# Kernel optimization log

Hardware: AMD Instinct MI355X
Metric: run time of the kernel (lower is better)

## Reference

```python
import jax, jax.numpy as jnp
import numpy as np

NUM_EXPERTS = 8
TOP_K = 2


def setup_inputs() -> dict:
    key = jax.random.key(0)
    ks = jax.random.split(key, 8)
    B = 16384
    D = 1024
    feat0 = jax.random.normal(ks[0], (B, 768), dtype=jnp.float32)
    feat1 = jax.random.normal(ks[1], (B, 512), dtype=jnp.float32)
    feat2 = jax.random.normal(ks[2], (B, 256), dtype=jnp.float32)
    # parameters (scaled like torch default init ~1/sqrt(fan_in))
    W_shared = jax.random.normal(ks[3], (1536, D), dtype=jnp.float32) * (1.0 / np.sqrt(1536))
    b_shared = jnp.zeros((D,), dtype=jnp.float32)
    W_gate = jax.random.normal(ks[4], (D, NUM_EXPERTS), dtype=jnp.float32) * (1.0 / np.sqrt(D))
    b_gate = jnp.zeros((NUM_EXPERTS,), dtype=jnp.float32)
    W_experts = jax.random.normal(ks[5], (NUM_EXPERTS, D, D), dtype=jnp.float32) * (1.0 / np.sqrt(D))
    b_experts = jnp.zeros((NUM_EXPERTS, D), dtype=jnp.float32)
    return {
        "feat0": feat0, "feat1": feat1, "feat2": feat2,
        "W_shared": W_shared, "b_shared": b_shared,
        "W_gate": W_gate, "b_gate": b_gate,
        "W_experts": W_experts, "b_experts": b_experts,
    }


def _moe_forward(feat0, feat1, feat2, W_shared, b_shared, W_gate, b_gate, W_experts, b_experts):
    x = jnp.concatenate([feat0, feat1, feat2], axis=1)          # (B, sum_d)
    h = jax.nn.gelu(x @ W_shared + b_shared, approximate=False)  # (B, D)
    gate_probs = jax.nn.softmax(h @ W_gate + b_gate, axis=-1)    # (B, E)
    topk_probs, topk_idx = jax.lax.top_k(gate_probs, TOP_K)      # (B, K)
    out = jnp.zeros_like(h)
    for e in range(NUM_EXPERTS):
        # per-token combine weight for expert e (0 if not routed to e)
        w_e = jnp.sum(topk_probs * (topk_idx == e), axis=1)      # (B,)
        expert_out = jax.nn.gelu(h @ W_experts[e] + b_experts[e], approximate=False)
        out = out + w_e[:, None] * expert_out
    return out


def reference(feat0, feat1, feat2, W_shared, b_shared, W_gate, b_gate, W_experts, b_experts):
    return _moe_forward(feat0, feat1, feat2, W_shared, b_shared, W_gate, b_gate, W_experts, b_experts)
```

## Files before the change

### kernel.cpp

```cpp
#include <hip/hip_runtime.h>
#include <math.h>

#define NB_TOK 16384
#define DM     1024
#define NEXP   8
#define KIN    1536

typedef __attribute__((ext_vector_type(8))) short          short8;
typedef __attribute__((ext_vector_type(8))) unsigned short ushort8;
typedef __attribute__((ext_vector_type(4))) unsigned short ushort4v;
typedef __attribute__((ext_vector_type(8))) _Float16       half8;
typedef __attribute__((ext_vector_type(4))) float          floatx4;

#define AS1U(p) ((const __attribute__((address_space(1))) unsigned int*)(p))
#define AS3U(p) ((__attribute__((address_space(3))) unsigned int*)(p))

__device__ __forceinline__ float gelu_f(float x) {
    return 0.5f * x * (1.0f + erff(x * 0.70710678118654752440f));
}

__device__ __forceinline__ unsigned short f2bf(float x) {
    unsigned u = __float_as_uint(x);
    u = (u + 0x7FFF + ((u >> 16) & 1)) >> 16;
    return (unsigned short)u;
}

__device__ __forceinline__ void split_h16(float x, unsigned short& hi, unsigned short& lo) {
    _Float16 h = (_Float16)x;
    float r = x - (float)h;
    _Float16 l = (_Float16)r;
    hi = *(unsigned short*)&h;
    lo = *(unsigned short*)&l;
}

__global__ __launch_bounds__(256) void k_splitA(
    const float* __restrict__ f0, const float* __restrict__ f1,
    const float* __restrict__ f2, unsigned short* __restrict__ Ah,
    unsigned short* __restrict__ Al)
{
    const int i4  = blockIdx.x * 256 + threadIdx.x;
    const int tok = i4 / (KIN / 4);
    const int k   = (i4 % (KIN / 4)) * 4;
    const float* src; int ld, c;
    if (k < 768)       { src = f0; ld = 768; c = k; }
    else if (k < 1280) { src = f1; ld = 512; c = k - 768; }
    else               { src = f2; ld = 256; c = k - 1280; }
    const float4 v = *(const float4*)(src + (size_t)tok * ld + c);
    const float* vp = (const float*)&v;
    ushort4v hi, lo;
#pragma unroll
    for (int j = 0; j < 4; ++j) {
        unsigned short h, l;
        split_h16(vp[j] * 4.0f, h, l);
        hi[j] = h; lo[j] = l;
    }
    *(ushort4v*)(Ah + (size_t)tok * KIN + k) = hi;
    *(ushort4v*)(Al + (size_t)tok * KIN + k) = lo;
}

__global__ __launch_bounds__(256) void k_splitB(
    const float* __restrict__ Ws, unsigned short* __restrict__ BhT,
    unsigned short* __restrict__ BlT)
{
    __shared__ float s[32][33];
    const int n0 = blockIdx.x * 32, k0 = blockIdx.y * 32;
    const int c  = threadIdx.x & 31, r = threadIdx.x >> 5;
#pragma unroll
    for (int p = 0; p < 4; ++p)
        s[r + p * 8][c] = Ws[(size_t)(k0 + r + p * 8) * DM + n0 + c];
    __syncthreads();
#pragma unroll
    for (int p = 0; p < 4; ++p) {
        const int n = r + p * 8;
        unsigned short h, l;
        split_h16(s[c][n] * 256.0f, h, l);
        BhT[(size_t)(n0 + n) * KIN + k0 + c] = h;
        BlT[(size_t)(n0 + n) * KIN + k0 + c] = l;
    }
}

__global__ __launch_bounds__(256) void k_shared_mfma(
    const unsigned short* __restrict__ Ah, const unsigned short* __restrict__ Al,
    const unsigned short* __restrict__ BhT, const unsigned short* __restrict__ BlT,
    const float* __restrict__ bs, float* __restrict__ h,
    unsigned short* __restrict__ hbf)
{
    __shared__ unsigned short ldsAh[128][64];
    __shared__ unsigned short ldsAl[128][64];
    __shared__ unsigned short ldsBh[128][64];
    __shared__ unsigned short ldsBl[128][64];

    const int t    = threadIdx.x;
    const int lane = t & 63;
    const int wave = t >> 6;
    const int row0 = blockIdx.y * 128;
    const int n0g  = blockIdx.x * 128;

    const int srow = t >> 3;
    const int g    = (t & 7) ^ (srow & 7);
    const unsigned short *sAh[4], *sAl[4], *sBh[4], *sBl[4];
#pragma unroll
    for (int q = 0; q < 4; ++q) {
        const size_t ra = (size_t)(row0 + q * 32 + srow) * KIN + g * 8;
        const size_t rb = (size_t)(n0g + q * 32 + srow) * KIN + g * 8;
        sAh[q] = Ah + ra; sAl[q] = Al + ra;
        sBh[q] = BhT + rb; sBl[q] = BlT + rb;
    }

    const int grp = lane >> 4;
    int offA[2][4], offB[2][4];
#pragma unroll
    for (int ks = 0; ks < 2; ++ks)
#pragma unroll
        for (int m = 0; m < 4; ++m) {
            const int rA = ((wave >> 1) * 64) + m * 16 + (lane & 15);
            const int rB = ((wave & 1) * 64) + m * 16 + (lane & 15);
            const int c  = ks * 4 + grp;
            offA[ks][m] = rA * 128 + (((c ^ (rA & 7)) & 7) << 4);
            offB[ks][m] = rB * 128 + (((c ^ (rB & 7)) & 7) << 4);
        }

    floatx4 acc[4][4];
#pragma unroll
    for (int m = 0; m < 4; ++m)
#pragma unroll
        for (int n = 0; n < 4; ++n) acc[m][n] = (floatx4){0.f, 0.f, 0.f, 0.f};

    const char* lAh = (const char*)&ldsAh[0][0];
    const char* lAl = (const char*)&ldsAl[0][0];
    const char* lBh = (const char*)&ldsBh[0][0];
    const char* lBl = (const char*)&ldsBl[0][0];

    for (int kt = 0; kt < KIN / 64; ++kt) {
        const int k0 = kt * 64;
        __syncthreads();
#pragma unroll
        for (int q = 0; q < 4; ++q) {
            const int dst = q * 4096 + wave * 1024;
            __builtin_amdgcn_global_load_lds(AS1U(sAh[q] + k0), AS3U((char*)lAh + dst), 16, 0, 0);
            __builtin_amdgcn_global_load_lds(AS1U(sAl[q] + k0), AS3U((char*)lAl + dst), 16, 0, 0);
            __builtin_amdgcn_global_load_lds(AS1U(sBh[q] + k0), AS3U((char*)lBh + dst), 16, 0, 0);
            __builtin_amdgcn_global_load_lds(AS1U(sBl[q] + k0), AS3U((char*)lBl + dst), 16, 0, 0);
        }
        __syncthreads();
#pragma unroll
        for (int ks = 0; ks < 2; ++ks) {
            half8 ah[4], al[4], bh[4], bl[4];
#pragma unroll
            for (int m = 0; m < 4; ++m) {
                ah[m] = *(const half8*)(lAh + offA[ks][m]);
                al[m] = *(const half8*)(lAl + offA[ks][m]);
            }
#pragma unroll
            for (int n = 0; n < 4; ++n) {
                bh[n] = *(const half8*)(lBh + offB[ks][n]);
                bl[n] = *(const half8*)(lBl + offB[ks][n]);
            }
#pragma unroll
            for (int m = 0; m < 4; ++m)
#pragma unroll
                for (int n = 0; n < 4; ++n) {
                    acc[m][n] = __builtin_amdgcn_mfma_f32_16x16x32_f16(ah[m], bh[n], acc[m][n], 0, 0, 0);
                    acc[m][n] = __builtin_amdgcn_mfma_f32_16x16x32_f16(ah[m], bl[n], acc[m][n], 0, 0, 0);
                    acc[m][n] = __builtin_amdgcn_mfma_f32_16x16x32_f16(al[m], bh[n], acc[m][n], 0, 0, 0);
                }
        }
    }

    const int wr = wave >> 1, wc = wave & 1;
#pragma unroll
    for (int n = 0; n < 4; ++n) {
        const int col  = n0g + wc * 64 + n * 16 + (lane & 15);
        const float bias = bs[col];
#pragma unroll
        for (int m = 0; m < 4; ++m) {
            const int rbase = row0 + wr * 64 + m * 16 + (lane >> 4) * 4;
#pragma unroll
            for (int reg = 0; reg < 4; ++reg) {
                const float o = gelu_f(acc[m][n][reg] * (1.0f / 1024.0f) + bias);
                h[(size_t)(rbase + reg) * DM + col]   = o;
                hbf[(size_t)(rbase + reg) * DM + col] = f2bf(o);
            }
        }
    }
}

__global__ __launch_bounds__(256) void k_wt_bf16(
    const float* __restrict__ We, unsigned short* __restrict__ WeT)
{
    __shared__ float s[32][33];
    const int e  = blockIdx.z;
    const int k0 = blockIdx.y * 32, n0 = blockIdx.x * 32;
    const int c  = threadIdx.x & 31, r = threadIdx.x >> 5;
    const float* W = We + ((size_t)e << 20);
#pragma unroll
    for (int p = 0; p < 4; ++p) {
        const int k = r + p * 8;
        s[k][c] = W[(size_t)(k0 + k) * DM + n0 + c];
    }
    __syncthreads();
#pragma unroll
    for (int p = 0; p < 4; ++p) {
        const int n = r + p * 8;
        WeT[((size_t)e << 20) + (size_t)(n0 + n) * DM + k0 + c] = f2bf(s[c][n]);
    }
}

__global__ __launch_bounds__(256) void k_gate_topk(
    const float* __restrict__ h, const float* __restrict__ Wg,
    const float* __restrict__ bg, int* __restrict__ eidx,
    float2* __restrict__ w01)
{
    const int lane = threadIdx.x & 63;
    const int wv   = threadIdx.x >> 6;
    const int tok  = blockIdx.x * 4 + wv;
    const float* hr = h + (size_t)tok * DM;
    float acc[NEXP];
#pragma unroll
    for (int e = 0; e < NEXP; ++e) acc[e] = 0.f;
    for (int j = 0; j < DM / 64; ++j) {
        const float hv = hr[lane + 64 * j];
        const float* wr = Wg + (size_t)(lane + 64 * j) * NEXP;
#pragma unroll
        for (int e = 0; e < NEXP; ++e) acc[e] = fmaf(hv, wr[e], acc[e]);
    }
#pragma unroll
    for (int off = 32; off > 0; off >>= 1) {
#pragma unroll
        for (int e = 0; e < NEXP; ++e) acc[e] += __shfl_xor(acc[e], off, 64);
    }
    if (lane == 0) {
        float lg[NEXP];
        float mx = -1e30f;
#pragma unroll
        for (int e = 0; e < NEXP; ++e) { lg[e] = acc[e] + bg[e]; mx = fmaxf(mx, lg[e]); }
        float p[NEXP]; float s = 0.f;
#pragma unroll
        for (int e = 0; e < NEXP; ++e) { p[e] = expf(lg[e] - mx); s += p[e]; }
        const float inv = 1.f / s;
        int i0 = 0;
#pragma unroll
        for (int e = 1; e < NEXP; ++e) if (p[e] > p[i0]) i0 = e;
        int i1 = (i0 == 0) ? 1 : 0;
#pragma unroll
        for (int e = 0; e < NEXP; ++e) if (e != i0 && p[e] > p[i1]) i1 = e;
        eidx[tok] = i0 | (i1 << 8);
        w01[tok]  = make_float2(p[i0] * inv, p[i1] * inv);
    }
}

__global__ __launch_bounds__(256) void k_bucket(
    const int* __restrict__ eidx, const float2* __restrict__ w01,
    int* __restrict__ counts, int* __restrict__ btok, float* __restrict__ bwgt,
    int2* __restrict__ tokslot)
{
    __shared__ int lcnt[NEXP], lbase[NEXP];
    const int tid = threadIdx.x;
    const int tok = blockIdx.x * 256 + tid;
    if (tid < NEXP) lcnt[tid] = 0;
    __syncthreads();
    const int ee = eidx[tok];
    const float2 w = w01[tok];
    const int e0 = ee & 0xff, e1 = ee >> 8;
    const int l0 = atomicAdd(&lcnt[e0], 1);
    const int l1 = atomicAdd(&lcnt[e1], 1);
    __syncthreads();
    if (tid < NEXP) lbase[tid] = atomicAdd(&counts[tid], lcnt[tid]);
    __syncthreads();
    const int s0 = lbase[e0] + l0;
    btok[e0 * NB_TOK + s0] = tok;  bwgt[e0 * NB_TOK + s0] = w.x;
    const int s1 = lbase[e1] + l1;
    btok[e1 * NB_TOK + s1] = tok;  bwgt[e1 * NB_TOK + s1] = w.y;
    tokslot[tok] = make_int2((e0 << 16) | s0, (e1 << 16) | s1);
}

__global__ void k_prefix(const int* __restrict__ counts, int* __restrict__ basep)
{
    if (threadIdx.x == 0) {
        int r = 0;
#pragma unroll
        for (int e = 0; e < NEXP; ++e) { basep[e] = r; r += counts[e]; }
    }
}

#define EXP_STAGE(b, k0)                                                                              \
    {                                                                                                 \
        char* lAw = (char*)&ldsA[b][0][0];                                                            \
        char* lBw = (char*)&ldsB[b][0][0];                                                            \
        _Pragma("unroll")                                                                             \
        for (int q = 0; q < 4; ++q) {                                                                 \
            __builtin_amdgcn_global_load_lds(AS1U(srcA[q] + (k0)), AS3U(lAw + q * 4096 + wave * 1024), 16, 0, 0); \
            __builtin_amdgcn_global_load_lds(AS1U(srcB[q] + (k0)), AS3U(lBw + q * 4096 + wave * 1024), 16, 0, 0); \
        }                                                                                             \
    }

__global__ __launch_bounds__(256) void k_expert_mfma(
    const unsigned short* __restrict__ hbf,
    const unsigned short* __restrict__ WeT,
    const float* __restrict__ bexp,
    const int* __restrict__ counts, const int* __restrict__ basep,
    const int* __restrict__ btok, const float* __restrict__ bwgt,
    float* __restrict__ stage)
{
    const int e    = blockIdx.z;
    const int cnt  = counts[e];
    const int row0 = blockIdx.y * 128;
    if (row0 >= cnt) return;
    const int gb   = basep[e];

    __shared__ unsigned short ldsA[2][128][64];
    __shared__ unsigned short ldsB[2][128][64];
    __shared__ int   sTok[128];
    __shared__ float sWt[128];

    const int t    = threadIdx.x;
    const int lane = t & 63;
    const int wave = t >> 6;

    if (t < 128) {
        const int idx = row0 + t;
        if (idx < cnt) { sTok[t] = btok[e * NB_TOK + idx]; sWt[t] = bwgt[e * NB_TOK + idx]; }
        else           { sTok[t] = -1;                     sWt[t] = 0.f; }
    }
    __syncthreads();

    const int srow = t >> 3;
    const int g    = (t & 7) ^ (srow & 7);
    const int n0g  = blockIdx.x * 128;
    const unsigned short* srcA[4];
    const unsigned short* srcB[4];
#pragma unroll
    for (int q = 0; q < 4; ++q) {
        int tk = sTok[q * 32 + srow];
        if (tk < 0) tk = 0;
        srcA[q] = hbf + (size_t)tk * DM + g * 8;
        srcB[q] = WeT + ((size_t)e << 20) + (size_t)(n0g + q * 32 + srow) * DM + g * 8;
    }

    const int grp = lane >> 4;
    int offA[2][4], offB[2][4];
#pragma unroll
    for (int ks = 0; ks < 2; ++ks)
#pragma unroll
        for (int m = 0; m < 4; ++m) {
            const int rA = ((wave >> 1) * 64) + m * 16 + (lane & 15);
            const int rB = ((wave & 1) * 64) + m * 16 + (lane & 15);
            const int c  = ks * 4 + grp;
            offA[ks][m] = rA * 128 + (((c ^ (rA & 7)) & 7) << 4);
            offB[ks][m] = rB * 128 + (((c ^ (rB & 7)) & 7) << 4);
        }

    floatx4 acc[4][4];
#pragma unroll
    for (int m = 0; m < 4; ++m)
#pragma unroll
        for (int n = 0; n < 4; ++n) acc[m][n] = (floatx4){0.f, 0.f, 0.f, 0.f};

    EXP_STAGE(0, 0);

    int buf = 0;
    for (int kt = 0; kt < DM / 64; ++kt) {
        __syncthreads();
        if (kt + 1 < DM / 64) EXP_STAGE(buf ^ 1, (kt + 1) * 64);
        const char* lA = (const char*)&ldsA[buf][0][0];
        const char* lB = (const char*)&ldsB[buf][0][0];
#pragma unroll
        for (int ks = 0; ks < 2; ++ks) {
            short8 av[4], bv[4];
#pragma unroll
            for (int m = 0; m < 4; ++m) av[m] = *(const short8*)(lA + offA[ks][m]);
#pragma unroll
            for (int n = 0; n < 4; ++n) bv[n] = *(const short8*)(lB + offB[ks][n]);
#pragma unroll
            for (int m = 0; m < 4; ++m)
#pragma unroll
                for (int n = 0; n < 4; ++n)
                    acc[m][n] = __builtin_amdgcn_mfma_f32_16x16x32_bf16(av[m], bv[n], acc[m][n], 0, 0, 0);
        }
        buf ^= 1;
    }

    const int wr = wave >> 1, wc = wave & 1;
#pragma unroll
    for (int n = 0; n < 4; ++n) {
        const int col  = n0g + wc * 64 + n * 16 + (lane & 15);
        const float bias = bexp[e * DM + col];
#pragma unroll
        for (int m = 0; m < 4; ++m) {
            const int rbase = wr * 64 + m * 16 + (lane >> 4) * 4;
#pragma unroll
            for (int reg = 0; reg < 4; ++reg) {
                const int r = rbase + reg;
                if (sTok[r] < 0) continue;
                const float v = gelu_f(acc[m][n][reg] + bias) * sWt[r];
                stage[(size_t)(gb + row0 + r) * DM + col] = v;
            }
        }
    }
}

__global__ __launch_bounds__(256) void k_combine(
    const float* __restrict__ stage, const int2* __restrict__ tokslot,
    const int* __restrict__ basep, float* __restrict__ out)
{
    const int tok = blockIdx.x;
    const int c   = threadIdx.x * 4;
    const int2 ts = tokslot[tok];
    const int g0 = basep[ts.x >> 16] + (ts.x & 0xFFFF);
    const int g1 = basep[ts.y >> 16] + (ts.y & 0xFFFF);
    const float4 a = *(const float4*)(stage + (size_t)g0 * DM + c);
    const float4 b = *(const float4*)(stage + (size_t)g1 * DM + c);
    float4 o;
    o.x = a.x + b.x; o.y = a.y + b.y; o.z = a.z + b.z; o.w = a.w + b.w;
    *(float4*)(out + (size_t)tok * DM + c) = o;
}

extern "C" void kernel_launch(void* const* d_in, const int* in_sizes, int n_in,
                              void* d_out, int out_size, void* d_ws, size_t ws_size,
                              hipStream_t stream)
{
    const float* f0 = (const float*)d_in[0];
    const float* f1 = (const float*)d_in[1];
    const float* f2 = (const float*)d_in[2];
    const float* Ws = (const float*)d_in[3];
    const float* bs = (const float*)d_in[4];
    const float* Wg = (const float*)d_in[5];
    const float* bg = (const float*)d_in[6];
    const float* We = (const float*)d_in[7];
    const float* be = (const float*)d_in[8];
    float* out = (float*)d_out;

    const size_t MB = 1048576ULL;
    char* base = (char*)d_ws;
    unsigned short* Ah   = (unsigned short*)(base);
    unsigned short* WeT  = (unsigned short*)(base);
    unsigned short* Al   = (unsigned short*)(base + 48 * MB);
    unsigned short* BhT  = (unsigned short*)(base + 96 * MB);
    unsigned short* BlT  = (unsigned short*)(base + 99 * MB);
    float*          h    = (float*)(base + 102 * MB);
    float*          stage= (float*)(base + 34 * MB);
    unsigned short* hbf  = (unsigned short*)(base + 166 * MB);
    int*    counts  = (int*)(base + 16 * MB);
    int*    basep   = counts + 16;
    int*    btok    = counts + 64;
    float*  bwgt    = (float*)(btok + NEXP * NB_TOK);
    int*    eidx    = (int*)(bwgt + NEXP * NB_TOK);
    float2* w01     = (float2*)(eidx + NB_TOK);
    int2*   tokslot = (int2*)(w01 + NB_TOK);

    k_splitA<<<NB_TOK * (KIN / 4) / 256, 256, 0, stream>>>(f0, f1, f2, Ah, Al);
    k_splitB<<<dim3(DM / 32, KIN / 32), 256, 0, stream>>>(Ws, BhT, BlT);
    k_shared_mfma<<<dim3(DM / 128, NB_TOK / 128), 256, 0, stream>>>(Ah, Al, BhT, BlT, bs, h, hbf);

    hipMemsetAsync(counts, 0, 16 * sizeof(int), stream);
    k_gate_topk<<<NB_TOK / 4, 256, 0, stream>>>(h, Wg, bg, eidx, w01);
    k_bucket<<<NB_TOK / 256, 256, 0, stream>>>(eidx, w01, counts, btok, bwgt, tokslot);
    k_prefix<<<1, 64, 0, stream>>>(counts, basep);

    k_wt_bf16<<<dim3(DM / 32, DM / 32, NEXP), 256, 0, stream>>>(We, WeT);

    k_expert_mfma<<<dim3(DM / 128, NB_TOK / 128, NEXP), 256, 0, stream>>>(
        hbf, WeT, be, counts, basep, btok, bwgt, stage);
    k_combine<<<NB_TOK, 256, 0, stream>>>(stage, tokslot, basep, out);
}
```

Before: 479.5 us.

## Pre-gather routed bf16 activations and scatter expert outputs directly by token

Adds a gather kernel that converts routed token rows of h to bf16 into a contiguous per-expert buffer. The expert GEMM then loads A rows contiguously and can issue its first async LDS stage before reading routing metadata. Expert outputs are written straight to out or a second-choice buffer keyed by token, which simplifies the combine and drops the tokslot indirection. The shared GEMM also gets a swizzled 1D block order for better L2 reuse. In exchange it adds an extra pass that reads h and writes a duplicated bf16 copy, and it drops the bf16 write from the shared GEMM epilogue.

Measured after the change: 491.1 us. 1.02x slower.

```diff
diff --git a/kernel.cpp b/kernel.cpp
--- a/kernel.cpp
+++ b/kernel.cpp
@@ -5,6 +5,8 @@
 #define DM     1024
 #define NEXP   8
 #define KIN    1536
+#define SECBIT 0x40000000
+#define TOKMSK 0x3FFFFFFF
 
 typedef __attribute__((ext_vector_type(8))) short          short8;
 typedef __attribute__((ext_vector_type(8))) unsigned short ushort8;
@@ -82,8 +84,7 @@
 __global__ __launch_bounds__(256) void k_shared_mfma(
     const unsigned short* __restrict__ Ah, const unsigned short* __restrict__ Al,
     const unsigned short* __restrict__ BhT, const unsigned short* __restrict__ BlT,
-    const float* __restrict__ bs, float* __restrict__ h,
-    unsigned short* __restrict__ hbf)
+    const float* __restrict__ bs, float* __restrict__ h)
 {
     __shared__ unsigned short ldsAh[128][64];
     __shared__ unsigned short ldsAl[128][64];
@@ -93,8 +94,11 @@
     const int t    = threadIdx.x;
     const int lane = t & 63;
     const int wave = t >> 6;
-    const int row0 = blockIdx.y * 128;
-    const int n0g  = blockIdx.x * 128;
+    const int bid  = blockIdx.x;
+    const int brow = ((bid >> 6) << 3) + (bid & 7);
+    const int bcol = (bid >> 3) & 7;
+    const int row0 = brow * 128;
+    const int n0g  = bcol * 128;
 
     const int srow = t >> 3;
     const int g    = (t & 7) ^ (srow & 7);
@@ -178,8 +182,7 @@
 #pragma unroll
             for (int reg = 0; reg < 4; ++reg) {
                 const float o = gelu_f(acc[m][n][reg] * (1.0f / 1024.0f) + bias);
-                h[(size_t)(rbase + reg) * DM + col]   = o;
-                hbf[(size_t)(rbase + reg) * DM + col] = f2bf(o);
+                h[(size_t)(rbase + reg) * DM + col] = o;
             }
         }
     }
@@ -251,8 +254,7 @@
 
 __global__ __launch_bounds__(256) void k_bucket(
     const int* __restrict__ eidx, const float2* __restrict__ w01,
-    int* __restrict__ counts, int* __restrict__ btok, float* __restrict__ bwgt,
-    int2* __restrict__ tokslot)
+    int* __restrict__ counts, int* __restrict__ btok, float* __restrict__ bwgt)
 {
     __shared__ int lcnt[NEXP], lbase[NEXP];
     const int tid = threadIdx.x;
@@ -268,10 +270,9 @@
     if (tid < NEXP) lbase[tid] = atomicAdd(&counts[tid], lcnt[tid]);
     __syncthreads();
     const int s0 = lbase[e0] + l0;
-    btok[e0 * NB_TOK + s0] = tok;  bwgt[e0 * NB_TOK + s0] = w.x;
+    btok[e0 * NB_TOK + s0] = tok;           bwgt[e0 * NB_TOK + s0] = w.x;
     const int s1 = lbase[e1] + l1;
-    btok[e1 * NB_TOK + s1] = tok;  bwgt[e1 * NB_TOK + s1] = w.y;
-    tokslot[tok] = make_int2((e0 << 16) | s0, (e1 << 16) | s1);
+    btok[e1 * NB_TOK + s1] = tok | SECBIT;  bwgt[e1 * NB_TOK + s1] = w.y;
 }
 
 __global__ void k_prefix(const int* __restrict__ counts, int* __restrict__ basep)
@@ -281,6 +282,23 @@
 #pragma unroll
         for (int e = 0; e < NEXP; ++e) { basep[e] = r; r += counts[e]; }
     }
+}
+
+__global__ __launch_bounds__(256) void k_gather(
+    const float* __restrict__ h, const int* __restrict__ btok,
+    const int* __restrict__ basep, unsigned short* __restrict__ hbfc)
+{
+    const int g = blockIdx.x;
+    int e = 0;
+#pragma unroll
+    for (int i = 1; i < NEXP; ++i) if (g >= basep[i]) e = i;
+    const int idx = g - basep[e];
+    const int tok = btok[e * NB_TOK + idx] & TOKMSK;
+    const int c   = threadIdx.x * 4;
+    const float4 v = *(const float4*)(h + (size_t)tok * DM + c);
+    ushort4v o;
+    o[0] = f2bf(v.x); o[1] = f2bf(v.y); o[2] = f2bf(v.z); o[3] = f2bf(v.w);
+    *(ushort4v*)(hbfc + (size_t)g * DM + c) = o;
 }
 
 #define EXP_STAGE(b, k0)                                                                              \
@@ -295,12 +313,12 @@
     }
 
 __global__ __launch_bounds__(256) void k_expert_mfma(
-    const unsigned short* __restrict__ hbf,
+    const unsigned short* __restrict__ hbfc,
     const unsigned short* __restrict__ WeT,
     const float* __restrict__ bexp,
     const int* __restrict__ counts, const int* __restrict__ basep,
     const int* __restrict__ btok, const float* __restrict__ bwgt,
-    float* __restrict__ stage)
+    float* __restrict__ stage2, float* __restrict__ out)
 {
     const int e    = blockIdx.z;
     const int cnt  = counts[e];
@@ -317,13 +335,6 @@
     const int lane = t & 63;
     const int wave = t >> 6;
 
-    if (t < 128) {
-        const int idx = row0 + t;
-        if (idx < cnt) { sTok[t] = btok[e * NB_TOK + idx]; sWt[t] = bwgt[e * NB_TOK + idx]; }
-        else           { sTok[t] = -1;                     sWt[t] = 0.f; }
-    }
-    __syncthreads();
-
     const int srow = t >> 3;
     const int g    = (t & 7) ^ (srow & 7);
     const int n0g  = blockIdx.x * 128;
@@ -331,10 +342,16 @@
     const unsigned short* srcB[4];
 #pragma unroll
     for (int q = 0; q < 4; ++q) {
-        int tk = sTok[q * 32 + srow];
-        if (tk < 0) tk = 0;
-        srcA[q] = hbf + (size_t)tk * DM + g * 8;
+        srcA[q] = hbfc + (size_t)(gb + row0 + q * 32 + srow) * DM + g * 8;
         srcB[q] = WeT + ((size_t)e << 20) + (size_t)(n0g + q * 32 + srow) * DM + g * 8;
+    }
+
+    EXP_STAGE(0, 0);
+
+    if (t < 128) {
+        const int idx = row0 + t;
+        if (idx < cnt) { sTok[t] = btok[e * NB_TOK + idx]; sWt[t] = bwgt[e * NB_TOK + idx]; }
+        else           { sTok[t] = 0;                      sWt[t] = 0.f; }
     }
 
     const int grp = lane >> 4;
@@ -356,8 +373,6 @@
 #pragma unroll
         for (int n = 0; n < 4; ++n) acc[m][n] = (floatx4){0.f, 0.f, 0.f, 0.f};
 
-    EXP_STAGE(0, 0);
-
     int buf = 0;
     for (int kt = 0; kt < DM / 64; ++kt) {
         __syncthreads();
@@ -391,25 +406,24 @@
 #pragma unroll
             for (int reg = 0; reg < 4; ++reg) {
                 const int r = rbase + reg;
-                if (sTok[r] < 0) continue;
+                if (row0 + r >= cnt) continue;
+                const int raw = sTok[r];
+                const int tok = raw & TOKMSK;
                 const float v = gelu_f(acc[m][n][reg] + bias) * sWt[r];
-                stage[(size_t)(gb + row0 + r) * DM + col] = v;
+                float* dst = (raw & SECBIT) ? stage2 : out;
+                dst[(size_t)tok * DM + col] = v;
             }
         }
     }
 }
 
 __global__ __launch_bounds__(256) void k_combine(
-    const float* __restrict__ stage, const int2* __restrict__ tokslot,
-    const int* __restrict__ basep, float* __restrict__ out)
+    const float* __restrict__ stage2, float* __restrict__ out)
 {
     const int tok = blockIdx.x;
     const int c   = threadIdx.x * 4;
-    const int2 ts = tokslot[tok];
-    const int g0 = basep[ts.x >> 16] + (ts.x & 0xFFFF);
-    const int g1 = basep[ts.y >> 16] + (ts.y & 0xFFFF);
-    const float4 a = *(const float4*)(stage + (size_t)g0 * DM + c);
-    const float4 b = *(const float4*)(stage + (size_t)g1 * DM + c);
+    const float4 a = *(const float4*)(out    + (size_t)tok * DM + c);
+    const float4 b = *(const float4*)(stage2 + (size_t)tok * DM + c);
     float4 o;
     o.x = a.x + b.x; o.y = a.y + b.y; o.z = a.z + b.z; o.w = a.w + b.w;
     *(float4*)(out + (size_t)tok * DM + c) = o;
@@ -432,34 +446,34 @@
 
     const size_t MB = 1048576ULL;
     char* base = (char*)d_ws;
-    unsigned short* Ah   = (unsigned short*)(base);
-    unsigned short* WeT  = (unsigned short*)(base);
-    unsigned short* Al   = (unsigned short*)(base + 48 * MB);
-    unsigned short* BhT  = (unsigned short*)(base + 96 * MB);
-    unsigned short* BlT  = (unsigned short*)(base + 99 * MB);
-    float*          h    = (float*)(base + 102 * MB);
-    float*          stage= (float*)(base + 34 * MB);
-    unsigned short* hbf  = (unsigned short*)(base + 166 * MB);
-    int*    counts  = (int*)(base + 16 * MB);
-    int*    basep   = counts + 16;
-    int*    btok    = counts + 64;
-    float*  bwgt    = (float*)(btok + NEXP * NB_TOK);
-    int*    eidx    = (int*)(bwgt + NEXP * NB_TOK);
-    float2* w01     = (float2*)(eidx + NB_TOK);
-    int2*   tokslot = (int2*)(w01 + NB_TOK);
+    unsigned short* Ah    = (unsigned short*)(base);
+    unsigned short* Al    = (unsigned short*)(base + 48 * MB);
+    unsigned short* BhT   = (unsigned short*)(base + 96 * MB);
+    unsigned short* BlT   = (unsigned short*)(base + 99 * MB);
+    float*          h     = (float*)(base + 102 * MB);
+    unsigned short* WeT   = (unsigned short*)(base + 2 * MB);
+    unsigned short* hbfc  = (unsigned short*)(base + 18 * MB);
+    float*          stage2= (float*)(base + 82 * MB);
+    int*    counts = (int*)(base);
+    int*    basep  = counts + 16;
+    int*    btok   = counts + 64;
+    float*  bwgt   = (float*)(btok + NEXP * NB_TOK);
+    int*    eidx   = (int*)(bwgt + NEXP * NB_TOK);
+    float2* w01    = (float2*)(eidx + NB_TOK);
 
     k_splitA<<<NB_TOK * (KIN / 4) / 256, 256, 0, stream>>>(f0, f1, f2, Ah, Al);
     k_splitB<<<dim3(DM / 32, KIN / 32), 256, 0, stream>>>(Ws, BhT, BlT);
-    k_shared_mfma<<<dim3(DM / 128, NB_TOK / 128), 256, 0, stream>>>(Ah, Al, BhT, BlT, bs, h, hbf);
+    k_shared_mfma<<<1024, 256, 0, stream>>>(Ah, Al, BhT, BlT, bs, h);
 
     hipMemsetAsync(counts, 0, 16 * sizeof(int), stream);
     k_gate_topk<<<NB_TOK / 4, 256, 0, stream>>>(h, Wg, bg, eidx, w01);
-    k_bucket<<<NB_TOK / 256, 256, 0, stream>>>(eidx, w01, counts, btok, bwgt, tokslot);
+    k_bucket<<<NB_TOK / 256, 256, 0, stream>>>(eidx, w01, counts, btok, bwgt);
     k_prefix<<<1, 64, 0, stream>>>(counts, basep);
+    k_gather<<<2 * NB_TOK, 256, 0, stream>>>(h, btok, basep, hbfc);
 
     k_wt_bf16<<<dim3(DM / 32, DM / 32, NEXP), 256, 0, stream>>>(We, WeT);
 
     k_expert_mfma<<<dim3(DM / 128, NB_TOK / 128, NEXP), 256, 0, stream>>>(
-        hbf, WeT, be, counts, basep, btok, bwgt, stage);
-    k_combine<<<NB_TOK, 256, 0, stream>>>(stage, tokslot, basep, out);
-}
+        hbfc, WeT, be, counts, basep, btok, bwgt, stage2, out);
+    k_combine<<<NB_TOK, 256, 0, stream>>>(stage2, out);
+}
```
